# Kernel optimization log

Measured on AMD Instinct MI355X. Metric: run time of the kernel, lower is better.

Reference implementation:

```python
import jax, jax.numpy as jnp
from jax import lax
import numpy as np

LEVELS = 3
HU_RANGE = 240.0 - (-160.0)          # hu_window = (-160, 240)
BASE_THR = 40.0 / HU_RANGE           # threshold / hu_range
MAD_TO_SIGMA = 1.0 / 0.6745


def haar2(x):
    """Single-level 2D orthonormal Haar DWT. x: [B, h, w] (h, w even).
    Returns cA, cH, cV, cD each [B, h//2, w//2]. Sign conventions are
    irrelevant to this loss (only |coeff| matters in MAD and L1 terms)."""
    B, h, w = x.shape
    x = x.reshape(B, h // 2, 2, w // 2, 2)
    a = x[:, :, 0, :, 0]
    b = x[:, :, 0, :, 1]
    c = x[:, :, 1, :, 0]
    d = x[:, :, 1, :, 1]
    cA = (a + b + c + d) * 0.5
    cH = (a + b - c - d) * 0.5
    cV = (a - b + c - d) * 0.5
    cD = (a - b - c + d) * 0.5
    return cA, cH, cV, cD


def soft_threshold(c, t):
    return jnp.sign(c) * jnp.maximum(jnp.abs(c) - t, 0.0)


def setup_inputs() -> dict:
    key = jax.random.key(0)
    pred = jax.random.normal(key, (128, 1, 512, 512), dtype=jnp.float32)
    return {"pred": pred}


def reference(pred):
    x = pred[:, 0]                     # [B, H, W]
    B = x.shape[0]

    # Multi-level decomposition: details[0] = finest, details[-1] = coarsest.
    details = []
    cA = x
    for _ in range(LEVELS):
        cA, cH, cV, cD = haar2(cA)
        details.append((cH, cV, cD))

    # pywt coeffs[1] is the COARSEST detail triple -> MAD noise estimate.
    cH, cV, cD = details[-1]
    all_details = jnp.concatenate(
        [cH.reshape(B, -1), cV.reshape(B, -1), cD.reshape(B, -1)], axis=1)
    sigma = jnp.median(jnp.abs(all_details), axis=1) * MAD_TO_SIGMA  # [B]
    adaptive_thr = jnp.clip(sigma * 2.5, BASE_THR * 0.5, BASE_THR * 2.0)
    adaptive_thr = lax.stop_gradient(adaptive_thr)                   # [B]

    # level_idx = 1 corresponds to pywt coeffs[1] (coarsest) = details[-1].
    total = jnp.zeros((B,), dtype=x.dtype)
    for level_idx in range(1, LEVELS + 1):
        cH, cV, cD = details[LEVELS - level_idx]
        t = (adaptive_thr / (2.0 ** (level_idx - 1)))[:, None, None]
        lvl = jnp.zeros((B,), dtype=x.dtype)
        for c in (cH, cV, cD):
            target = lax.stop_gradient(soft_threshold(c, t))
            lvl = lvl + jnp.mean(jnp.abs(c - target), axis=(1, 2))
        total = total + (1.0 / level_idx) * lvl / 3.0

    loss = jnp.mean(total)             # sum over batch / valid_samples (all valid)
    avg_noise = jnp.mean(sigma)
    return loss, avg_noise
```

## Files before the change

kernel.cpp:

```cpp
#include <hip/hip_runtime.h>
#include <stdint.h>


static constexpr int BATCH = 128;
static constexpr int W = 512;
static constexpr int NBIN = 512;

__device__ __forceinline__ float block_reduce_sum(float v, float* lds) {
    #pragma unroll
    for (int off = 32; off > 0; off >>= 1)
        v += __shfl_down(v, off, 64);
    const int lane = threadIdx.x & 63;
    const int wave = threadIdx.x >> 6;
    if (lane == 0) lds[wave] = v;
    __syncthreads();
    if (threadIdx.x == 0) {
        float s = 0.0f;
        for (int w = 0; w < 4; ++w) s += lds[w];
        lds[0] = s;
    }
    __syncthreads();
    const float r = lds[0];
    __syncthreads();
    return r;
}

__device__ __forceinline__ void haar_quad(float a, float b, float c, float d,
                                          float& cA, float& cH, float& cV, float& cD) {
    const float sab = a + b, scd = c + d, dab = a - b, dcd = c - d;
    cA = 0.5f * (sab + scd);
    cH = 0.5f * (sab - scd);
    cV = 0.5f * (dab + dcd);
    cD = 0.5f * (dab - dcd);
}

__device__ __forceinline__ float wavelet_block_loss(
        const float* __restrict__ blk, float t1, float t2, float t3) {
    float cA1[4][4];
    float s1 = 0.0f, s2 = 0.0f, s3 = 0.0f;
    #pragma unroll
    for (int rr = 0; rr < 4; ++rr) {
        const float4 r0a = *(const float4*)(blk + (size_t)(2 * rr) * W);
        const float4 r0b = *(const float4*)(blk + (size_t)(2 * rr) * W + 4);
        const float4 r1a = *(const float4*)(blk + (size_t)(2 * rr + 1) * W);
        const float4 r1b = *(const float4*)(blk + (size_t)(2 * rr + 1) * W + 4);
        const float top[8] = {r0a.x, r0a.y, r0a.z, r0a.w, r0b.x, r0b.y, r0b.z, r0b.w};
        const float bot[8] = {r1a.x, r1a.y, r1a.z, r1a.w, r1b.x, r1b.y, r1b.z, r1b.w};
        #pragma unroll
        for (int cc = 0; cc < 4; ++cc) {
            float cA, cH, cV, cD;
            haar_quad(top[2*cc], top[2*cc+1], bot[2*cc], bot[2*cc+1], cA, cH, cV, cD);
            s1 += fminf(fabsf(cH), t1) + fminf(fabsf(cV), t1) + fminf(fabsf(cD), t1);
            cA1[rr][cc] = cA;
        }
    }
    float cA2[2][2];
    #pragma unroll
    for (int rr = 0; rr < 2; ++rr)
        #pragma unroll
        for (int cc = 0; cc < 2; ++cc) {
            float cA, cH, cV, cD;
            haar_quad(cA1[2*rr][2*cc], cA1[2*rr][2*cc+1],
                      cA1[2*rr+1][2*cc], cA1[2*rr+1][2*cc+1], cA, cH, cV, cD);
            s2 += fminf(fabsf(cH), t2) + fminf(fabsf(cV), t2) + fminf(fabsf(cD), t2);
            cA2[rr][cc] = cA;
        }
    {
        float cA, cH, cV, cD;
        haar_quad(cA2[0][0], cA2[0][1], cA2[1][0], cA2[1][1], cA, cH, cV, cD);
        s3 = fminf(fabsf(cH), t3) + fminf(fabsf(cV), t3) + fminf(fabsf(cD), t3);
    }
    const float w1 = 1.0f / (9.0f * 65536.0f);
    const float w2 = 1.0f / (6.0f * 16384.0f);
    const float w3 = 1.0f / (3.0f * 4096.0f);
    return s1 * w1 + s2 * w2 + s3 * w3;
}

__global__ __launch_bounds__(256) void pass_a(const float* __restrict__ x,
                                              float* __restrict__ partials,
                                              uint32_t* __restrict__ ghist,
                                              float* __restrict__ out) {
    __shared__ uint32_t h[NBIN];
    __shared__ float lds[8];
    const int tid  = threadIdx.x;
    const int lane = tid & 63;
    const int wv   = tid >> 6;
    const int sub  = blockIdx.x;
    const int b    = blockIdx.y;

    h[tid] = 0u;
    h[tid + 256] = 0u;
    if (sub == 0 && b == 0 && tid < 2) out[tid] = 0.0f;
    __syncthreads();

    const float BASE = 40.0f / 400.0f;
    const float t3 = BASE * 2.0f, t2 = t3 * 0.5f, t1 = t3 * 0.25f;

    const int R = sub * 4 + wv;
    const float* strip = x + (size_t)b * W * W + (size_t)(R * 8) * W;

    float cA1A[4][2], cA1B[4][2];
    float s1 = 0.0f, s2 = 0.0f, s3 = 0.0f;

    #pragma unroll
    for (int half = 0; half < 2; ++half) {
        float4 ld[2][4];
        #pragma unroll
        for (int q = 0; q < 2; ++q) {
            const int rp = half * 2 + q;
            const float* r0 = strip + (size_t)(2 * rp) * W;
            const float* r1 = strip + (size_t)(2 * rp + 1) * W;
            ld[q][0] = *(const float4*)(r0 + 4 * lane);
            ld[q][1] = *(const float4*)(r1 + 4 * lane);
            ld[q][2] = *(const float4*)(r0 + 256 + 4 * lane);
            ld[q][3] = *(const float4*)(r1 + 256 + 4 * lane);
        }
        #pragma unroll
        for (int q = 0; q < 2; ++q) {
            const int rp = half * 2 + q;
            const float4 tA = ld[q][0], bA = ld[q][1];
            const float4 tB = ld[q][2], bB = ld[q][3];

            float cA, cH, cV, cD;
            haar_quad(tA.x, tA.y, bA.x, bA.y, cA, cH, cV, cD);
            s1 += fminf(fabsf(cH), t1) + fminf(fabsf(cV), t1) + fminf(fabsf(cD), t1);
            cA1A[rp][0] = cA;
            haar_quad(tA.z, tA.w, bA.z, bA.w, cA, cH, cV, cD);
            s1 += fminf(fabsf(cH), t1) + fminf(fabsf(cV), t1) + fminf(fabsf(cD), t1);
            cA1A[rp][1] = cA;
            haar_quad(tB.x, tB.y, bB.x, bB.y, cA, cH, cV, cD);
            s1 += fminf(fabsf(cH), t1) + fminf(fabsf(cV), t1) + fminf(fabsf(cD), t1);
            cA1B[rp][0] = cA;
            haar_quad(tB.z, tB.w, bB.z, bB.w, cA, cH, cV, cD);
            s1 += fminf(fabsf(cH), t1) + fminf(fabsf(cV), t1) + fminf(fabsf(cD), t1);
            cA1B[rp][1] = cA;
        }
    }

    float cA2A[2], cA2B[2];
    #pragma unroll
    for (int j = 0; j < 2; ++j) {
        float cA, cH, cV, cD;
        haar_quad(cA1A[2*j][0], cA1A[2*j][1], cA1A[2*j+1][0], cA1A[2*j+1][1],
                  cA, cH, cV, cD);
        s2 += fminf(fabsf(cH), t2) + fminf(fabsf(cV), t2) + fminf(fabsf(cD), t2);
        cA2A[j] = cA;
        haar_quad(cA1B[2*j][0], cA1B[2*j][1], cA1B[2*j+1][0], cA1B[2*j+1][1],
                  cA, cH, cV, cD);
        s2 += fminf(fabsf(cH), t2) + fminf(fabsf(cV), t2) + fminf(fabsf(cD), t2);
        cA2B[j] = cA;
    }

    {
        const float send0 = (lane & 1) ? cA2A[0] : cA2B[0];
        const float send1 = (lane & 1) ? cA2A[1] : cA2B[1];
        const float p0 = __shfl_xor(send0, 1, 64);
        const float p1 = __shfl_xor(send1, 1, 64);
        const float q0 = (lane & 1) ? cA2B[0] : cA2A[0];
        const float q2 = (lane & 1) ? cA2B[1] : cA2A[1];
        float cA, cH, cV, cD;
        haar_quad(q0, p0, q2, p1, cA, cH, cV, cD);
        const float aH = fabsf(cH), aV = fabsf(cV), aD = fabsf(cD);
        s3 += fminf(aH, t3) + fminf(aV, t3) + fminf(aD, t3);
        atomicAdd(&h[min((int)(aH * 256.0f), NBIN - 1)], 1u);
        atomicAdd(&h[min((int)(aV * 256.0f), NBIN - 1)], 1u);
        atomicAdd(&h[min((int)(aD * 256.0f), NBIN - 1)], 1u);
    }

    const float w1 = 1.0f / (9.0f * 65536.0f);
    const float w2 = 1.0f / (6.0f * 16384.0f);
    const float w3 = 1.0f / (3.0f * 4096.0f);
    const float part = s1 * w1 + s2 * w2 + s3 * w3;

    const float tot = block_reduce_sum(part, lds);
    if (tid == 0) partials[b * 16 + sub] = tot;

    uint32_t* gh = ghist + ((size_t)b * 16 + sub) * NBIN;
    gh[tid] = h[tid];
    gh[tid + 256] = h[tid + 256];
}

__global__ __launch_bounds__(64) void pass_b(const uint32_t* __restrict__ ghist,
                                             const float* __restrict__ partials,
                                             const float* __restrict__ x,
                                             float* __restrict__ out) {
    const int b = blockIdx.x;
    const int lane = threadIdx.x;

    const float pval = (lane < 16) ? partials[b * 16 + lane] : 0.0f;

    uint32_t c[8] = {0, 0, 0, 0, 0, 0, 0, 0};

    #pragma unroll
    for (int s = 0; s < 16; ++s) {
        const uint32_t* hb = ghist + ((size_t)b * 16 + s) * NBIN + lane * 8;
        const uint4 u0 = *(const uint4*)(hb);
        const uint4 u1 = *(const uint4*)(hb + 4);
        c[0] += u0.x; c[1] += u0.y; c[2] += u0.z; c[3] += u0.w;
        c[4] += u1.x; c[5] += u1.y; c[6] += u1.z; c[7] += u1.w;
    }

    uint32_t lane_sum = 0;
    #pragma unroll
    for (int j = 0; j < 8; ++j) lane_sum += c[j];

    uint32_t incl = lane_sum;
    #pragma unroll
    for (int off = 1; off < 64; off <<= 1) {
        const uint32_t v = __shfl_up(incl, off, 64);
        if (lane >= off) incl += v;
    }
    uint32_t run = incl - lane_sum;

    int bin1 = 0x7FFFFFFF, bin2 = 0x7FFFFFFF;
    #pragma unroll
    for (int j = 0; j < 8; ++j) {
        const uint32_t nxt = run + c[j];
        if (run < 6144u && nxt >= 6144u) bin1 = lane * 8 + j;
        if (run < 6145u && nxt >= 6145u) bin2 = lane * 8 + j;
        run = nxt;
    }
    #pragma unroll
    for (int off = 32; off > 0; off >>= 1) {
        bin1 = min(bin1, __shfl_down(bin1, off, 64));
        bin2 = min(bin2, __shfl_down(bin2, off, 64));
    }
    bin1 = __shfl(bin1, 0, 64);
    bin2 = __shfl(bin2, 0, 64);

    const float v1 = ((float)bin1 + 0.5f) * (1.0f / 256.0f);
    const float v2 = ((float)bin2 + 0.5f) * (1.0f / 256.0f);
    const float med = 0.5f * (v1 + v2);
    const float sig = med * (float)(1.0 / 0.6745);
    const float BASE = 40.0f / 400.0f;
    const float TTOP = BASE * 2.0f;
    const float t = fminf(fmaxf(sig * 2.5f, BASE * 0.5f), TTOP);

    float loss_b;
    if (t == TTOP) {
        float v = pval;
        #pragma unroll
        for (int off = 32; off > 0; off >>= 1) v += __shfl_down(v, off, 64);
        loss_b = v;
    } else {
        float part = 0.0f;
        #pragma unroll 1
        for (int k = 0; k < 64; ++k) {
            const int p = k * 64 + lane;
            const int i3 = p >> 6, j3 = p & 63;
            const float* blk = x + (size_t)b * W * W + (size_t)(i3 * 8) * W + j3 * 8;
            part += wavelet_block_loss(blk, t * 0.25f, t * 0.5f, t);
        }
        #pragma unroll
        for (int off = 32; off > 0; off >>= 1) part += __shfl_down(part, off, 64);
        loss_b = part;
    }

    if (lane == 0) {
        atomicAdd(&out[0], loss_b * (1.0f / (float)BATCH));
        atomicAdd(&out[1], sig * (1.0f / (float)BATCH));
    }
}

extern "C" void kernel_launch(void* const* d_in, const int* in_sizes, int n_in,
                              void* d_out, int out_size, void* d_ws, size_t ws_size,
                              hipStream_t stream) {
    const float* x = (const float*)d_in[0];
    float* ws = (float*)d_ws;
    float* partials = ws;
    uint32_t* ghist = (uint32_t*)(ws + 2048);

    dim3 grid(16, BATCH);
    pass_a<<<grid, 256, 0, stream>>>(x, partials, ghist, (float*)d_out);
    pass_b<<<BATCH, 64, 0, stream>>>(ghist, partials, x, (float*)d_out);
}
```

Baseline: 191.1 us.

## Fuse histogram-median pass into main kernel via last-block-done atomics

Merges the two kernels into one. The last block to finish for each batch image, detected with an atomic counter, does the histogram merge, median, threshold and per-image loss. A final global counter lets the last image's block write the batch means deterministically. This removes the second kernel launch and its dependency gap, but adds a memset launch, threadfences and atomic counters.

```diff
diff --git a/kernel.cpp b/kernel.cpp
--- a/kernel.cpp
+++ b/kernel.cpp
@@ -76,12 +76,17 @@
     return s1 * w1 + s2 * w2 + s3 * w3;
 }
 
-__global__ __launch_bounds__(256) void pass_a(const float* __restrict__ x,
-                                              float* __restrict__ partials,
-                                              uint32_t* __restrict__ ghist,
-                                              float* __restrict__ out) {
+__global__ __launch_bounds__(256) void fused(const float* __restrict__ x,
+                                             float* __restrict__ partials,
+                                             uint32_t* __restrict__ ghist,
+                                             uint32_t* __restrict__ cnt,
+                                             uint32_t* __restrict__ done,
+                                             float* __restrict__ loss_arr,
+                                             float* __restrict__ sig_arr,
+                                             float* __restrict__ out) {
     __shared__ uint32_t h[NBIN];
     __shared__ float lds[8];
+    __shared__ uint32_t flag;
     const int tid  = threadIdx.x;
     const int lane = tid & 63;
     const int wv   = tid >> 6;
@@ -90,7 +95,6 @@
 
     h[tid] = 0u;
     h[tid + 256] = 0u;
-    if (sub == 0 && b == 0 && tid < 2) out[tid] = 0.0f;
     __syncthreads();
 
     const float BASE = 40.0f / 400.0f;
@@ -178,87 +182,108 @@
     uint32_t* gh = ghist + ((size_t)b * 16 + sub) * NBIN;
     gh[tid] = h[tid];
     gh[tid + 256] = h[tid + 256];
-}
-
-__global__ __launch_bounds__(64) void pass_b(const uint32_t* __restrict__ ghist,
-                                             const float* __restrict__ partials,
-                                             const float* __restrict__ x,
-                                             float* __restrict__ out) {
-    const int b = blockIdx.x;
-    const int lane = threadIdx.x;
-
-    const float pval = (lane < 16) ? partials[b * 16 + lane] : 0.0f;
-
-    uint32_t c[8] = {0, 0, 0, 0, 0, 0, 0, 0};
-
-    #pragma unroll
-    for (int s = 0; s < 16; ++s) {
-        const uint32_t* hb = ghist + ((size_t)b * 16 + s) * NBIN + lane * 8;
-        const uint4 u0 = *(const uint4*)(hb);
-        const uint4 u1 = *(const uint4*)(hb + 4);
-        c[0] += u0.x; c[1] += u0.y; c[2] += u0.z; c[3] += u0.w;
-        c[4] += u1.x; c[5] += u1.y; c[6] += u1.z; c[7] += u1.w;
-    }
-
-    uint32_t lane_sum = 0;
-    #pragma unroll
-    for (int j = 0; j < 8; ++j) lane_sum += c[j];
-
-    uint32_t incl = lane_sum;
-    #pragma unroll
-    for (int off = 1; off < 64; off <<= 1) {
-        const uint32_t v = __shfl_up(incl, off, 64);
-        if (lane >= off) incl += v;
-    }
-    uint32_t run = incl - lane_sum;
-
-    int bin1 = 0x7FFFFFFF, bin2 = 0x7FFFFFFF;
-    #pragma unroll
-    for (int j = 0; j < 8; ++j) {
-        const uint32_t nxt = run + c[j];
-        if (run < 6144u && nxt >= 6144u) bin1 = lane * 8 + j;
-        if (run < 6145u && nxt >= 6145u) bin2 = lane * 8 + j;
-        run = nxt;
-    }
-    #pragma unroll
-    for (int off = 32; off > 0; off >>= 1) {
-        bin1 = min(bin1, __shfl_down(bin1, off, 64));
-        bin2 = min(bin2, __shfl_down(bin2, off, 64));
-    }
-    bin1 = __shfl(bin1, 0, 64);
-    bin2 = __shfl(bin2, 0, 64);
-
-    const float v1 = ((float)bin1 + 0.5f) * (1.0f / 256.0f);
-    const float v2 = ((float)bin2 + 0.5f) * (1.0f / 256.0f);
-    const float med = 0.5f * (v1 + v2);
-    const float sig = med * (float)(1.0 / 0.6745);
-    const float BASE = 40.0f / 400.0f;
-    const float TTOP = BASE * 2.0f;
-    const float t = fminf(fmaxf(sig * 2.5f, BASE * 0.5f), TTOP);
-
-    float loss_b;
-    if (t == TTOP) {
-        float v = pval;
-        #pragma unroll
-        for (int off = 32; off > 0; off >>= 1) v += __shfl_down(v, off, 64);
-        loss_b = v;
-    } else {
-        float part = 0.0f;
-        #pragma unroll 1
-        for (int k = 0; k < 64; ++k) {
-            const int p = k * 64 + lane;
-            const int i3 = p >> 6, j3 = p & 63;
-            const float* blk = x + (size_t)b * W * W + (size_t)(i3 * 8) * W + j3 * 8;
-            part += wavelet_block_loss(blk, t * 0.25f, t * 0.5f, t);
-        }
-        #pragma unroll
-        for (int off = 32; off > 0; off >>= 1) part += __shfl_down(part, off, 64);
-        loss_b = part;
-    }
-
-    if (lane == 0) {
-        atomicAdd(&out[0], loss_b * (1.0f / (float)BATCH));
-        atomicAdd(&out[1], sig * (1.0f / (float)BATCH));
+
+    __threadfence();
+    __syncthreads();
+    if (tid == 0)
+        flag = (atomicAdd(&cnt[b], 1u) == 15u) ? 1u : 0u;
+    __syncthreads();
+    if (flag == 0u) return;
+
+    if (tid >= 64) return;
+    __threadfence();
+    {
+        const int ln = tid;
+
+        const float pval = (ln < 16) ? partials[b * 16 + ln] : 0.0f;
+
+        uint32_t c[8] = {0, 0, 0, 0, 0, 0, 0, 0};
+        #pragma unroll
+        for (int s = 0; s < 16; ++s) {
+            const uint32_t* hb = ghist + ((size_t)b * 16 + s) * NBIN + ln * 8;
+            const uint4 u0 = *(const uint4*)(hb);
+            const uint4 u1 = *(const uint4*)(hb + 4);
+            c[0] += u0.x; c[1] += u0.y; c[2] += u0.z; c[3] += u0.w;
+            c[4] += u1.x; c[5] += u1.y; c[6] += u1.z; c[7] += u1.w;
+        }
+
+        uint32_t lane_sum = 0;
+        #pragma unroll
+        for (int j = 0; j < 8; ++j) lane_sum += c[j];
+
+        uint32_t incl = lane_sum;
+        #pragma unroll
+        for (int off = 1; off < 64; off <<= 1) {
+            const uint32_t v = __shfl_up(incl, off, 64);
+            if (ln >= off) incl += v;
+        }
+        uint32_t run = incl - lane_sum;
+
+        int bin1 = 0x7FFFFFFF, bin2 = 0x7FFFFFFF;
+        #pragma unroll
+        for (int j = 0; j < 8; ++j) {
+            const uint32_t nxt = run + c[j];
+            if (run < 6144u && nxt >= 6144u) bin1 = ln * 8 + j;
+            if (run < 6145u && nxt >= 6145u) bin2 = ln * 8 + j;
+            run = nxt;
+        }
+        #pragma unroll
+        for (int off = 32; off > 0; off >>= 1) {
+            bin1 = min(bin1, __shfl_down(bin1, off, 64));
+            bin2 = min(bin2, __shfl_down(bin2, off, 64));
+        }
+        bin1 = __shfl(bin1, 0, 64);
+        bin2 = __shfl(bin2, 0, 64);
+
+        const float v1 = ((float)bin1 + 0.5f) * (1.0f / 256.0f);
+        const float v2 = ((float)bin2 + 0.5f) * (1.0f / 256.0f);
+        const float med = 0.5f * (v1 + v2);
+        const float sig = med * (float)(1.0 / 0.6745);
+        const float TTOP = BASE * 2.0f;
+        const float t = fminf(fmaxf(sig * 2.5f, BASE * 0.5f), TTOP);
+
+        float loss_b;
+        if (t == TTOP) {
+            float v = pval;
+            #pragma unroll
+            for (int off = 32; off > 0; off >>= 1) v += __shfl_down(v, off, 64);
+            loss_b = v;
+        } else {
+            float prt = 0.0f;
+            #pragma unroll 1
+            for (int k = 0; k < 64; ++k) {
+                const int p = k * 64 + ln;
+                const int i3 = p >> 6, j3 = p & 63;
+                const float* blk = x + (size_t)b * W * W + (size_t)(i3 * 8) * W + j3 * 8;
+                prt += wavelet_block_loss(blk, t * 0.25f, t * 0.5f, t);
+            }
+            #pragma unroll
+            for (int off = 32; off > 0; off >>= 1) prt += __shfl_down(prt, off, 64);
+            loss_b = prt;
+        }
+
+        uint32_t dold = 0u;
+        if (ln == 0) {
+            loss_arr[b] = loss_b;
+            sig_arr[b]  = sig;
+            __threadfence();
+            dold = atomicAdd(done, 1u);
+        }
+        dold = (uint32_t)__shfl((int)dold, 0, 64);
+        if (dold == (uint32_t)(BATCH - 1)) {
+            __threadfence();
+            float va = loss_arr[ln] + loss_arr[ln + 64];
+            float vs = sig_arr[ln]  + sig_arr[ln + 64];
+            #pragma unroll
+            for (int off = 32; off > 0; off >>= 1) {
+                va += __shfl_down(va, off, 64);
+                vs += __shfl_down(vs, off, 64);
+            }
+            if (ln == 0) {
+                out[0] = va * (1.0f / (float)BATCH);
+                out[1] = vs * (1.0f / (float)BATCH);
+            }
+        }
     }
 }
 
@@ -269,8 +294,14 @@
     float* ws = (float*)d_ws;
     float* partials = ws;
     uint32_t* ghist = (uint32_t*)(ws + 2048);
+    uint32_t* cnt   = ghist + (size_t)BATCH * 16 * NBIN;
+    uint32_t* done  = cnt + BATCH;
+    float* loss_arr = (float*)(done + 1);
+    float* sig_arr  = loss_arr + BATCH;
+
+    hipMemsetAsync(cnt, 0, (BATCH + 1) * sizeof(uint32_t), stream);
 
     dim3 grid(16, BATCH);
-    pass_a<<<grid, 256, 0, stream>>>(x, partials, ghist, (float*)d_out);
-    pass_b<<<BATCH, 64, 0, stream>>>(ghist, partials, x, (float*)d_out);
-}
+    fused<<<grid, 256, 0, stream>>>(x, partials, ghist, cnt, done,
+                                    loss_arr, sig_arr, (float*)d_out);
+}
```

After: 562.1 us. 194% more time.
